# Kernel tuning notes

Hardware: AMD Instinct MI355X
Metric: run time of the kernel (lower is better)

## Reference

```python
import jax, jax.numpy as jnp
import numpy as np

N_NODES = 50000
N_EDGES = 600000
NUM_FILTERS = 128
HIDDEN = 128
LOG2 = float(np.log(2.0))
EPS = 1e-5


def _xavier(key, fan_out, fan_in):
    bound = float(np.sqrt(6.0 / (fan_in + fan_out)))
    return jax.random.uniform(key, (fan_out, fan_in), jnp.float32, -bound, bound)


def setup_inputs() -> dict:
    key = jax.random.key(0)
    k = jax.random.split(key, 6)
    v = jax.random.normal(k[0], (N_NODES, HIDDEN), jnp.float32)
    e = jax.random.normal(k[1], (N_EDGES, NUM_FILTERS), jnp.float32)
    edge_index = jax.random.randint(k[2], (2, N_EDGES), 0, N_NODES, jnp.int64 if jax.config.jax_enable_x64 else jnp.int32)
    return {
        "v": v,
        "e": e,
        "edge_index": edge_index,
        "v1_size": 30000,
        "W11": _xavier(k[3], HIDDEN, NUM_FILTERS),
        "b11": jnp.zeros((HIDDEN,), jnp.float32),
        "W12": _xavier(k[4], HIDDEN, HIDDEN),
        "b12": jnp.zeros((HIDDEN,), jnp.float32),
        "ln_w": jnp.ones((HIDDEN,), jnp.float32),
        "ln_b": jnp.zeros((HIDDEN,), jnp.float32),
    }


def shifted_softplus(x):
    return jax.nn.softplus(x) - LOG2


def reference(v, e, edge_index, v1_size, W11, b11, W12, b12, ln_w, ln_b):
    # scatter-sum edge features onto destination nodes (edge_index[1])
    i = edge_index[1]
    agg = jax.ops.segment_sum(e, i, num_segments=v.shape[0])  # [N, F]
    # original splits at v1_size but uses the SAME lin1_1/lin1_2 on both
    # halves, so applying to the full tensor is mathematically identical.
    h = shifted_softplus(agg @ W11.T + b11) @ W12.T + b12  # [N, H]
    mu = jnp.mean(h, axis=-1, keepdims=True)
    var = jnp.mean(jnp.square(h - mu), axis=-1, keepdims=True)
    out = (h - mu) * jax.lax.rsqrt(var + EPS) * ln_w + ln_b
    return v + out
```

## Files before the change

### kernel.cpp

```cpp
#include <hip/hip_runtime.h>
#include <math.h>

#define NN 50000
#define NE 600000
#define CAP 64
#define LOG2C 0.69314718055994530942f
#define EPSC 1e-5f


__global__ void k_bucket(const int4* __restrict__ dst4, int* __restrict__ cursor,
                         int* __restrict__ buckets) {
  int i = blockIdx.x * blockDim.x + threadIdx.x;
  if (i < NE / 4) {
    int4 d = dst4[i];
    int s0 = atomicAdd(&cursor[d.x], 1); if (s0 < CAP) buckets[d.x * CAP + s0] = 4 * i + 0;
    int s1 = atomicAdd(&cursor[d.y], 1); if (s1 < CAP) buckets[d.y * CAP + s1] = 4 * i + 1;
    int s2 = atomicAdd(&cursor[d.z], 1); if (s2 < CAP) buckets[d.z * CAP + s2] = 4 * i + 2;
    int s3 = atomicAdd(&cursor[d.w], 1); if (s3 < CAP) buckets[d.w * CAP + s3] = 4 * i + 3;
  }
}


__global__ __launch_bounds__(256)
void k_gather(const float* __restrict__ e, const int* __restrict__ cursor,
              const int* __restrict__ buckets, float* __restrict__ agg) {
  const int node = (int)((blockIdx.x * 256u + threadIdx.x) >> 6);
  const int lane = threadIdx.x & 63;
  if (node >= NN) return;
  int deg = cursor[node];
  deg = deg < CAP ? deg : CAP;
  const int* bk = buckets + node * CAP;
  const float2* e2 = (const float2*)e;

  float2 a0 = make_float2(0.f, 0.f), a1 = a0, a2 = a0, a3 = a0;
  int j = 0;
  for (; j + 4 <= deg; j += 4) {
    int4 id = *(const int4*)(bk + j);
    float2 x0 = e2[id.x * 64 + lane];
    float2 x1 = e2[id.y * 64 + lane];
    float2 x2 = e2[id.z * 64 + lane];
    float2 x3 = e2[id.w * 64 + lane];
    a0.x += x0.x; a0.y += x0.y;
    a1.x += x1.x; a1.y += x1.y;
    a2.x += x2.x; a2.y += x2.y;
    a3.x += x3.x; a3.y += x3.y;
  }
  if (j + 2 <= deg) {
    int i0 = bk[j], i1 = bk[j + 1];
    float2 x0 = e2[i0 * 64 + lane];
    float2 x1 = e2[i1 * 64 + lane];
    a0.x += x0.x; a0.y += x0.y;
    a1.x += x1.x; a1.y += x1.y;
    j += 2;
  }
  if (j < deg) {
    int i0 = bk[j];
    float2 x = e2[i0 * 64 + lane];
    a0.x += x.x; a0.y += x.y;
  }
  float2 r;
  r.x = (a0.x + a1.x) + (a2.x + a3.x);
  r.y = (a0.y + a1.y) + (a2.y + a3.y);
  ((float2*)agg)[node * 64 + lane] = r;
}


__device__ __forceinline__ float sspf(float x) {
  return fmaxf(x, 0.f) + log1pf(expf(-fabsf(x))) - LOG2C;
}

__global__ __launch_bounds__(256, 4)
void k_mlp(float* aggout,
           const float* __restrict__ v,
           const float* __restrict__ W11, const float* __restrict__ b11,
           const float* __restrict__ W12, const float* __restrict__ b12,
           const float* __restrict__ lnw, const float* __restrict__ lnb) {
  __shared__ float smem[64 * 128];
  float4* smem4 = (float4*)smem;
  const int tid  = threadIdx.x;
  const int tx   = tid & 15;
  const int ty   = tid >> 4;
  const int lane = tid & 63;
  const int wv   = tid >> 6;
  const int node0 = blockIdx.x * 64;
  const int wrow0 = wv * 16;

  if (node0 + wrow0 >= NN) return;

  {
    const float4* ag4 = (const float4*)aggout;
    #pragma unroll
    for (int t4 = 0; t4 < 8; ++t4) {
      const int t = t4 * 64 + lane;
      const int row = t >> 5;
      const int g   = t & 31;
      float4 val = ag4[(size_t)(node0 + wrow0 + row) * 32 + g];
      const int gp = g ^ (((wrow0 + row) >> 2) & 7);
      smem4[(wrow0 + row) * 32 + gp] = val;
    }
  }

  const int r0 = ty * 4;
  const int sw = ty & 7;
  const int cb = tx * 8;
  float acc[4][8];

  {
    const float4 bb0 = ((const float4*)b11)[tx * 2];
    const float4 bb1 = ((const float4*)b11)[tx * 2 + 1];
    #pragma unroll
    for (int i = 0; i < 4; ++i) {
      acc[i][0] = bb0.x; acc[i][1] = bb0.y; acc[i][2] = bb0.z; acc[i][3] = bb0.w;
      acc[i][4] = bb1.x; acc[i][5] = bb1.y; acc[i][6] = bb1.z; acc[i][7] = bb1.w;
    }
    const float4* Wg = (const float4*)W11;
    #pragma unroll 2
    for (int k4 = 0; k4 < 32; ++k4) {
      const int kk = k4 ^ sw;
      float4 a[4];
      #pragma unroll
      for (int i = 0; i < 4; ++i) a[i] = smem4[(r0 + i) * 32 + kk];
      float4 w[8];
      #pragma unroll
      for (int j = 0; j < 8; ++j) w[j] = Wg[(cb + j) * 32 + k4];
      #pragma unroll
      for (int i = 0; i < 4; ++i)
        #pragma unroll
        for (int j = 0; j < 8; ++j)
          acc[i][j] = fmaf(a[i].x, w[j].x, fmaf(a[i].y, w[j].y,
                      fmaf(a[i].z, w[j].z, fmaf(a[i].w, w[j].w, acc[i][j]))));
    }
    #pragma unroll
    for (int i = 0; i < 4; ++i) {
      #pragma unroll
      for (int j4 = 0; j4 < 2; ++j4) {
        float4 h;
        h.x = sspf(acc[i][j4 * 4 + 0]);
        h.y = sspf(acc[i][j4 * 4 + 1]);
        h.z = sspf(acc[i][j4 * 4 + 2]);
        h.w = sspf(acc[i][j4 * 4 + 3]);
        const int gp = (tx * 2 + j4) ^ sw;
        smem4[(r0 + i) * 32 + gp] = h;
      }
    }
  }

  {
    const float4 bb0 = ((const float4*)b12)[tx * 2];
    const float4 bb1 = ((const float4*)b12)[tx * 2 + 1];
    #pragma unroll
    for (int i = 0; i < 4; ++i) {
      acc[i][0] = bb0.x; acc[i][1] = bb0.y; acc[i][2] = bb0.z; acc[i][3] = bb0.w;
      acc[i][4] = bb1.x; acc[i][5] = bb1.y; acc[i][6] = bb1.z; acc[i][7] = bb1.w;
    }
    const float4* Wg = (const float4*)W12;
    #pragma unroll 2
    for (int k4 = 0; k4 < 32; ++k4) {
      const int kk = k4 ^ sw;
      float4 a[4];
      #pragma unroll
      for (int i = 0; i < 4; ++i) a[i] = smem4[(r0 + i) * 32 + kk];
      float4 w[8];
      #pragma unroll
      for (int j = 0; j < 8; ++j) w[j] = Wg[(cb + j) * 32 + k4];
      #pragma unroll
      for (int i = 0; i < 4; ++i)
        #pragma unroll
        for (int j = 0; j < 8; ++j)
          acc[i][j] = fmaf(a[i].x, w[j].x, fmaf(a[i].y, w[j].y,
                      fmaf(a[i].z, w[j].z, fmaf(a[i].w, w[j].w, acc[i][j]))));
    }
  }

  {
    const float4 lw0 = ((const float4*)lnw)[tx * 2];
    const float4 lw1 = ((const float4*)lnw)[tx * 2 + 1];
    const float4 lb0 = ((const float4*)lnb)[tx * 2];
    const float4 lb1 = ((const float4*)lnb)[tx * 2 + 1];
    #pragma unroll
    for (int i = 0; i < 4; ++i) {
      const int row = node0 + r0 + i;
      float s = 0.f, ss = 0.f;
      #pragma unroll
      for (int j = 0; j < 8; ++j) { s += acc[i][j]; ss = fmaf(acc[i][j], acc[i][j], ss); }
      #pragma unroll
      for (int m = 8; m >= 1; m >>= 1) {
        s  += __shfl_xor(s, m, 64);
        ss += __shfl_xor(ss, m, 64);
      }
      const float mu   = s * (1.0f / 128.0f);
      const float varr = fmaxf(ss * (1.0f / 128.0f) - mu * mu, 0.f);
      const float rstd = rsqrtf(varr + EPSC);
      const float4 v0 = ((const float4*)v)[(size_t)row * 32 + tx * 2];
      const float4 v1 = ((const float4*)v)[(size_t)row * 32 + tx * 2 + 1];
      float4 o0, o1;
      o0.x = fmaf((acc[i][0] - mu) * rstd, lw0.x, lb0.x) + v0.x;
      o0.y = fmaf((acc[i][1] - mu) * rstd, lw0.y, lb0.y) + v0.y;
      o0.z = fmaf((acc[i][2] - mu) * rstd, lw0.z, lb0.z) + v0.z;
      o0.w = fmaf((acc[i][3] - mu) * rstd, lw0.w, lb0.w) + v0.w;
      o1.x = fmaf((acc[i][4] - mu) * rstd, lw1.x, lb1.x) + v1.x;
      o1.y = fmaf((acc[i][5] - mu) * rstd, lw1.y, lb1.y) + v1.y;
      o1.z = fmaf((acc[i][6] - mu) * rstd, lw1.z, lb1.z) + v1.z;
      o1.w = fmaf((acc[i][7] - mu) * rstd, lw1.w, lb1.w) + v1.w;
      ((float4*)aggout)[(size_t)row * 32 + tx * 2]     = o0;
      ((float4*)aggout)[(size_t)row * 32 + tx * 2 + 1] = o1;
    }
  }
}


extern "C" void kernel_launch(void* const* d_in, const int* in_sizes, int n_in,
                              void* d_out, int out_size, void* d_ws, size_t ws_size,
                              hipStream_t stream) {
  const float* v   = (const float*)d_in[0];
  const float* e   = (const float*)d_in[1];
  const int*   ei  = (const int*)d_in[2];
  const float* W11 = (const float*)d_in[4];
  const float* b11 = (const float*)d_in[5];
  const float* W12 = (const float*)d_in[6];
  const float* b12 = (const float*)d_in[7];
  const float* lnw = (const float*)d_in[8];
  const float* lnb = (const float*)d_in[9];
  float* out = (float*)d_out;

  int* cursor  = (int*)d_ws;
  int* buckets = cursor + 50048;

  const int4* dst4 = (const int4*)(ei + NE);

  hipMemsetAsync(cursor, 0, NN * sizeof(int), stream);
  k_bucket<<<(NE / 4 + 255) / 256, 256, 0, stream>>>(dst4, cursor, buckets);
  k_gather<<<(NN * 64 + 255) / 256, 256, 0, stream>>>(e, cursor, buckets, out);
  k_mlp<<<(NN + 63) / 64, 256, 0, stream>>>(out, v, W11, b11, W12, b12, lnw, lnb);
}
```

Before: 722.6 us.

## Make MLP kernel persistent with both weight matrices staged in LDS

The MLP kernel becomes a persistent kernel of 256 blocks with 512 threads. Each block loads W11 and W12 once into 160KB of swizzled dynamic LDS. Waves then claim 8-row tiles through an atomic work counter and run both layers out of LDS instead of rereading the weights from global memory. This removes repeated global weight traffic and per-block setup. In exchange it runs one block per CU, with only two rows per thread in the register tile, and depends on the MI355X LDS capacity allowing a 160KB allocation.

```diff
diff --git a/kernel.cpp b/kernel.cpp
--- a/kernel.cpp
+++ b/kernel.cpp
@@ -4,6 +4,7 @@
 #define NN 50000
 #define NE 600000
 #define CAP 64
+#define NT8 6250
 #define LOG2C 0.69314718055994530942f
 #define EPSC 1e-5f
 
@@ -69,120 +70,115 @@
   return fmaxf(x, 0.f) + log1pf(expf(-fabsf(x))) - LOG2C;
 }
 
-__global__ __launch_bounds__(256, 4)
+__global__ __launch_bounds__(512, 1)
 void k_mlp(float* aggout,
            const float* __restrict__ v,
            const float* __restrict__ W11, const float* __restrict__ b11,
            const float* __restrict__ W12, const float* __restrict__ b12,
-           const float* __restrict__ lnw, const float* __restrict__ lnb) {
-  __shared__ float smem[64 * 128];
-  float4* smem4 = (float4*)smem;
-  const int tid  = threadIdx.x;
-  const int tx   = tid & 15;
-  const int ty   = tid >> 4;
+           const float* __restrict__ lnw, const float* __restrict__ lnb,
+           int* __restrict__ ctr) {
+  extern __shared__ float smem[];
+  float4* sW1 = (float4*)smem;
+  float4* sW2 = sW1 + 4096;
+  float4* sA  = sW2 + 4096;
+
+  const int tid = threadIdx.x;
+
+  {
+    const float4* W1g = (const float4*)W11;
+    const float4* W2g = (const float4*)W12;
+    #pragma unroll
+    for (int i4 = tid; i4 < 4096; i4 += 512) {
+      int row = i4 >> 5, k4 = i4 & 31;
+      int slot = (row << 5) | (k4 ^ ((row >> 3) & 7));
+      sW1[slot] = W1g[i4];
+      sW2[slot] = W2g[i4];
+    }
+  }
+  __syncthreads();
+
   const int lane = tid & 63;
   const int wv   = tid >> 6;
-  const int node0 = blockIdx.x * 64;
-  const int wrow0 = wv * 16;
-
-  if (node0 + wrow0 >= NN) return;
-
-  {
-    const float4* ag4 = (const float4*)aggout;
-    #pragma unroll
-    for (int t4 = 0; t4 < 8; ++t4) {
-      const int t = t4 * 64 + lane;
-      const int row = t >> 5;
-      const int g   = t & 31;
-      float4 val = ag4[(size_t)(node0 + wrow0 + row) * 32 + g];
-      const int gp = g ^ (((wrow0 + row) >> 2) & 7);
-      smem4[(wrow0 + row) * 32 + gp] = val;
-    }
-  }
-
-  const int r0 = ty * 4;
-  const int sw = ty & 7;
-  const int cb = tx * 8;
-  float acc[4][8];
-
-  {
-    const float4 bb0 = ((const float4*)b11)[tx * 2];
-    const float4 bb1 = ((const float4*)b11)[tx * 2 + 1];
-    #pragma unroll
-    for (int i = 0; i < 4; ++i) {
-      acc[i][0] = bb0.x; acc[i][1] = bb0.y; acc[i][2] = bb0.z; acc[i][3] = bb0.w;
-      acc[i][4] = bb1.x; acc[i][5] = bb1.y; acc[i][6] = bb1.z; acc[i][7] = bb1.w;
-    }
-    const float4* Wg = (const float4*)W11;
-    #pragma unroll 2
+  const int tx   = tid & 15;
+  const int ty   = (tid >> 4) & 3;
+  const int cb   = tx * 8;
+  const int kw   = tx & 7;
+  const int la   = ty * 2, lb = ty * 2 + 1;
+  float4* sAw = sA + wv * 256;
+
+  float bias1[8], bias2[8], lwv[8], lbv[8];
+  #pragma unroll
+  for (int j = 0; j < 8; ++j) {
+    bias1[j] = b11[cb + j];
+    bias2[j] = b12[cb + j];
+    lwv[j]   = lnw[cb + j];
+    lbv[j]   = lnb[cb + j];
+  }
+
+  const float4* ag4 = (const float4*)aggout;
+
+  for (;;) {
+    int t8;
+    if (lane == 0) t8 = atomicAdd(ctr, 1);
+    t8 = __shfl(t8, 0, 64);
+    if (t8 >= NT8) break;
+    const int row0 = t8 * 8;
+
+    #pragma unroll
+    for (int q = 0; q < 4; ++q) {
+      int tt = q * 64 + lane;
+      int lr = tt >> 5, g = tt & 31;
+      sAw[(lr << 5) | (g ^ lr)] = ag4[(size_t)(row0 + lr) * 32 + g];
+    }
+
+    float acc0[8], acc1[8];
+
+    #pragma unroll
+    for (int j = 0; j < 8; ++j) { acc0[j] = bias1[j]; acc1[j] = bias1[j]; }
+    #pragma unroll 4
     for (int k4 = 0; k4 < 32; ++k4) {
-      const int kk = k4 ^ sw;
-      float4 a[4];
-      #pragma unroll
-      for (int i = 0; i < 4; ++i) a[i] = smem4[(r0 + i) * 32 + kk];
-      float4 w[8];
-      #pragma unroll
-      for (int j = 0; j < 8; ++j) w[j] = Wg[(cb + j) * 32 + k4];
-      #pragma unroll
-      for (int i = 0; i < 4; ++i)
-        #pragma unroll
-        for (int j = 0; j < 8; ++j)
-          acc[i][j] = fmaf(a[i].x, w[j].x, fmaf(a[i].y, w[j].y,
-                      fmaf(a[i].z, w[j].z, fmaf(a[i].w, w[j].w, acc[i][j]))));
-    }
-    #pragma unroll
-    for (int i = 0; i < 4; ++i) {
-      #pragma unroll
-      for (int j4 = 0; j4 < 2; ++j4) {
-        float4 h;
-        h.x = sspf(acc[i][j4 * 4 + 0]);
-        h.y = sspf(acc[i][j4 * 4 + 1]);
-        h.z = sspf(acc[i][j4 * 4 + 2]);
-        h.w = sspf(acc[i][j4 * 4 + 3]);
-        const int gp = (tx * 2 + j4) ^ sw;
-        smem4[(r0 + i) * 32 + gp] = h;
+      float4 a0 = sAw[(la << 5) | (k4 ^ la)];
+      float4 a1 = sAw[(lb << 5) | (k4 ^ lb)];
+      #pragma unroll
+      for (int j = 0; j < 8; ++j) {
+        float4 w = sW1[((cb + j) << 5) | (k4 ^ kw)];
+        acc0[j] = fmaf(a0.x, w.x, fmaf(a0.y, w.y, fmaf(a0.z, w.z, fmaf(a0.w, w.w, acc0[j]))));
+        acc1[j] = fmaf(a1.x, w.x, fmaf(a1.y, w.y, fmaf(a1.z, w.z, fmaf(a1.w, w.w, acc1[j]))));
       }
     }
-  }
-
-  {
-    const float4 bb0 = ((const float4*)b12)[tx * 2];
-    const float4 bb1 = ((const float4*)b12)[tx * 2 + 1];
-    #pragma unroll
-    for (int i = 0; i < 4; ++i) {
-      acc[i][0] = bb0.x; acc[i][1] = bb0.y; acc[i][2] = bb0.z; acc[i][3] = bb0.w;
-      acc[i][4] = bb1.x; acc[i][5] = bb1.y; acc[i][6] = bb1.z; acc[i][7] = bb1.w;
-    }
-    const float4* Wg = (const float4*)W12;
-    #pragma unroll 2
+
+    #pragma unroll
+    for (int j4 = 0; j4 < 2; ++j4) {
+      float4 h0, h1;
+      h0.x = sspf(acc0[j4 * 4 + 0]); h0.y = sspf(acc0[j4 * 4 + 1]);
+      h0.z = sspf(acc0[j4 * 4 + 2]); h0.w = sspf(acc0[j4 * 4 + 3]);
+      h1.x = sspf(acc1[j4 * 4 + 0]); h1.y = sspf(acc1[j4 * 4 + 1]);
+      h1.z = sspf(acc1[j4 * 4 + 2]); h1.w = sspf(acc1[j4 * 4 + 3]);
+      sAw[(la << 5) | ((tx * 2 + j4) ^ la)] = h0;
+      sAw[(lb << 5) | ((tx * 2 + j4) ^ lb)] = h1;
+    }
+
+    #pragma unroll
+    for (int j = 0; j < 8; ++j) { acc0[j] = bias2[j]; acc1[j] = bias2[j]; }
+    #pragma unroll 4
     for (int k4 = 0; k4 < 32; ++k4) {
-      const int kk = k4 ^ sw;
-      float4 a[4];
-      #pragma unroll
-      for (int i = 0; i < 4; ++i) a[i] = smem4[(r0 + i) * 32 + kk];
-      float4 w[8];
-      #pragma unroll
-      for (int j = 0; j < 8; ++j) w[j] = Wg[(cb + j) * 32 + k4];
-      #pragma unroll
-      for (int i = 0; i < 4; ++i)
-        #pragma unroll
-        for (int j = 0; j < 8; ++j)
-          acc[i][j] = fmaf(a[i].x, w[j].x, fmaf(a[i].y, w[j].y,
-                      fmaf(a[i].z, w[j].z, fmaf(a[i].w, w[j].w, acc[i][j]))));
-    }
-  }
-
-  {
-    const float4 lw0 = ((const float4*)lnw)[tx * 2];
-    const float4 lw1 = ((const float4*)lnw)[tx * 2 + 1];
-    const float4 lb0 = ((const float4*)lnb)[tx * 2];
-    const float4 lb1 = ((const float4*)lnb)[tx * 2 + 1];
-    #pragma unroll
-    for (int i = 0; i < 4; ++i) {
-      const int row = node0 + r0 + i;
+      float4 a0 = sAw[(la << 5) | (k4 ^ la)];
+      float4 a1 = sAw[(lb << 5) | (k4 ^ lb)];
+      #pragma unroll
+      for (int j = 0; j < 8; ++j) {
+        float4 w = sW2[((cb + j) << 5) | (k4 ^ kw)];
+        acc0[j] = fmaf(a0.x, w.x, fmaf(a0.y, w.y, fmaf(a0.z, w.z, fmaf(a0.w, w.w, acc0[j]))));
+        acc1[j] = fmaf(a1.x, w.x, fmaf(a1.y, w.y, fmaf(a1.z, w.z, fmaf(a1.w, w.w, acc1[j]))));
+      }
+    }
+
+    #pragma unroll
+    for (int i = 0; i < 2; ++i) {
+      float* ac = i ? acc1 : acc0;
+      const int gr = row0 + ty * 2 + i;
       float s = 0.f, ss = 0.f;
       #pragma unroll
-      for (int j = 0; j < 8; ++j) { s += acc[i][j]; ss = fmaf(acc[i][j], acc[i][j], ss); }
+      for (int j = 0; j < 8; ++j) { s += ac[j]; ss = fmaf(ac[j], ac[j], ss); }
       #pragma unroll
       for (int m = 8; m >= 1; m >>= 1) {
         s  += __shfl_xor(s, m, 64);
@@ -191,19 +187,19 @@
       const float mu   = s * (1.0f / 128.0f);
       const float varr = fmaxf(ss * (1.0f / 128.0f) - mu * mu, 0.f);
       const float rstd = rsqrtf(varr + EPSC);
-      const float4 v0 = ((const float4*)v)[(size_t)row * 32 + tx * 2];
-      const float4 v1 = ((const float4*)v)[(size_t)row * 32 + tx * 2 + 1];
+      const float4 v0 = ((const float4*)v)[(size_t)gr * 32 + tx * 2];
+      const float4 v1 = ((const float4*)v)[(size_t)gr * 32 + tx * 2 + 1];
       float4 o0, o1;
-      o0.x = fmaf((acc[i][0] - mu) * rstd, lw0.x, lb0.x) + v0.x;
-      o0.y = fmaf((acc[i][1] - mu) * rstd, lw0.y, lb0.y) + v0.y;
-      o0.z = fmaf((acc[i][2] - mu) * rstd, lw0.z, lb0.z) + v0.z;
-      o0.w = fmaf((acc[i][3] - mu) * rstd, lw0.w, lb0.w) + v0.w;
-      o1.x = fmaf((acc[i][4] - mu) * rstd, lw1.x, lb1.x) + v1.x;
-      o1.y = fmaf((acc[i][5] - mu) * rstd, lw1.y, lb1.y) + v1.y;
-      o1.z = fmaf((acc[i][6] - mu) * rstd, lw1.z, lb1.z) + v1.z;
-      o1.w = fmaf((acc[i][7] - mu) * rstd, lw1.w, lb1.w) + v1.w;
-      ((float4*)aggout)[(size_t)row * 32 + tx * 2]     = o0;
-      ((float4*)aggout)[(size_t)row * 32 + tx * 2 + 1] = o1;
+      o0.x = fmaf((ac[0] - mu) * rstd, lwv[0], lbv[0]) + v0.x;
+      o0.y = fmaf((ac[1] - mu) * rstd, lwv[1], lbv[1]) + v0.y;
+      o0.z = fmaf((ac[2] - mu) * rstd, lwv[2], lbv[2]) + v0.z;
+      o0.w = fmaf((ac[3] - mu) * rstd, lwv[3], lbv[3]) + v0.w;
+      o1.x = fmaf((ac[4] - mu) * rstd, lwv[4], lbv[4]) + v1.x;
+      o1.y = fmaf((ac[5] - mu) * rstd, lwv[5], lbv[5]) + v1.y;
+      o1.z = fmaf((ac[6] - mu) * rstd, lwv[6], lbv[6]) + v1.z;
+      o1.w = fmaf((ac[7] - mu) * rstd, lwv[7], lbv[7]) + v1.w;
+      ((float4*)aggout)[(size_t)gr * 32 + tx * 2]     = o0;
+      ((float4*)aggout)[(size_t)gr * 32 + tx * 2 + 1] = o1;
     }
   }
 }
@@ -224,12 +220,15 @@
   float* out = (float*)d_out;
 
   int* cursor  = (int*)d_ws;
+  int* ctr     = cursor + NN;
   int* buckets = cursor + 50048;
 
   const int4* dst4 = (const int4*)(ei + NE);
 
-  hipMemsetAsync(cursor, 0, NN * sizeof(int), stream);
+  hipMemsetAsync(cursor, 0, 50048 * sizeof(int), stream);
   k_bucket<<<(NE / 4 + 255) / 256, 256, 0, stream>>>(dst4, cursor, buckets);
   k_gather<<<(NN * 64 + 255) / 256, 256, 0, stream>>>(e, cursor, buckets, out);
-  k_mlp<<<(NN + 63) / 64, 256, 0, stream>>>(out, v, W11, b11, W12, b12, lnw, lnb);
-}
+
+  hipFuncSetAttribute((const void*)k_mlp, hipFuncAttributeMaxDynamicSharedMemorySize, 163840);
+  k_mlp<<<256, 512, 163840, stream>>>(out, v, W11, b11, W12, b12, lnw, lnb, ctr);
+}
```

Result: faster. 622.6 us (-13.8%).
